# Performance work log

Measured on AMD Instinct MI355X. Metric: run time of the kernel, lower is better.

The kernel has to match this reference:

```python
import jax, jax.numpy as jnp
import numpy as np

N_SPLIT = 4096   # split tokens (coarse octree levels)
N_VQ    = 12288  # VQ tokens (finest level)
N       = N_SPLIT + N_VQ
C       = 256    # num_embed
H       = 8      # num_heads
L       = 4      # num_blocks
P       = 256    # patch_size (attention window)
DIL     = 2      # dilation for odd (swin) blocks
DVQ     = 32     # vqvae embedding_channels
VQ_SIZE = 256    # vqvae embedding_sizes
VQ_G    = 4      # vqvae quantizer_group
HID     = 4 * C


def _layernorm(x, s, b):
    m = x.mean(-1, keepdims=True)
    v = jnp.var(x, axis=-1, keepdims=True)
    return (x - m) * jax.lax.rsqrt(v + 1e-5) * s + b


def _sin_pos_emb(n, c):
    pos = jnp.arange(n, dtype=jnp.float32)[:, None]
    half = c // 2
    freqs = jnp.exp(-jnp.log(10000.0) * jnp.arange(half, dtype=jnp.float32) / half)
    ang = pos * freqs
    return jnp.concatenate([jnp.sin(ang), jnp.cos(ang)], axis=-1)


def _forward(split, zq, targets_vq, category, batch_id, mask, d2b,
             split_emb, class_emb, vq_proj_w, vq_proj_b,
             ln1_s, ln1_b, qkv_w, qkv_b, attn_w, attn_b,
             ln2_s, ln2_b, fc1_w, fc1_b, fc2_w, fc2_b,
             lnx_s, lnx_b, split_w, split_b, vq_w, vq_b):
    # token embeddings: [split tokens ; projected VQ codes]
    x = jnp.concatenate([split_emb[split], zq @ vq_proj_w + vq_proj_b], axis=0)  # [N,C]
    cond = class_emb[category]                      # [B,C]
    x = jnp.where(mask[:, None], cond[batch_id], x)  # masked tokens -> class cond

    # depth2batch gather, then OctFormer blocks
    xb = x[d2b] + _sin_pos_emb(N, C).astype(x.dtype)
    dh = C // H
    scale = dh ** -0.5
    for l in range(L):
        d = DIL if (l % 2 == 1) else 1  # swin-style alternating dilation
        h = _layernorm(xb, ln1_s[l], ln1_b[l])
        # dilated window partition: window j in a super-window holds tokens base+p*d+j
        hw = h.reshape(-1, P, d, C).transpose(0, 2, 1, 3).reshape(-1, P, C)
        qkv = hw @ qkv_w[l] + qkv_b[l]              # [nw,P,3C]
        q, k, v = [t.reshape(-1, P, H, dh) for t in jnp.split(qkv, 3, axis=-1)]
        att = jax.nn.softmax(jnp.einsum('wphd,wqhd->whpq', q, k) * scale, axis=-1)
        o = jnp.einsum('whpq,wqhd->wphd', att, v).reshape(-1, P, C) @ attn_w[l] + attn_b[l]
        o = o.reshape(-1, d, P, C).transpose(0, 2, 1, 3).reshape(-1, C)  # undo partition
        xb = xb + o
        h = _layernorm(xb, ln2_s[l], ln2_b[l])
        xb = xb + (jax.nn.gelu(h @ fc1_w[l] + fc1_b[l]) @ fc2_w[l] + fc2_b[l])
    # batch2depth scatter (inverse permutation)
    x = jnp.zeros_like(xb).at[d2b].set(xb)
    x = _layernorm(x, lnx_s, lnx_b)

    # split head + masked cross-entropy
    sl = x[:N_SPLIT] @ split_w + split_b            # [Ns,2]
    ms = mask[:N_SPLIT].astype(jnp.float32)
    ce_s = -jnp.take_along_axis(jax.nn.log_softmax(sl, axis=-1), split[:, None], axis=-1)[:, 0]
    split_loss = jnp.sum(ce_s * ms) / jnp.maximum(jnp.sum(ms), 1.0)

    # vq head + masked grouped cross-entropy
    vl = (x[N_SPLIT:] @ vq_w + vq_b).reshape(N_VQ, VQ_G, VQ_SIZE)
    mv = mask[N_SPLIT:].astype(jnp.float32)
    ce_v = -jnp.take_along_axis(jax.nn.log_softmax(vl, axis=-1), targets_vq[..., None], axis=-1)[..., 0]
    vq_loss = jnp.sum(ce_v.mean(-1) * mv) / jnp.maximum(jnp.sum(mv), 1.0)
    return jnp.stack([split_loss, vq_loss])


def setup_inputs() -> dict:
    key = jax.random.key(0)
    ks = jax.random.split(key, 16)
    s = 0.02
    inp = {
        'split': jax.random.randint(ks[0], (N_SPLIT,), 0, 2),
        'zq': jax.random.normal(ks[1], (N_VQ, DVQ), jnp.float32),
        'targets_vq': jax.random.randint(ks[2], (N_VQ, VQ_G), 0, VQ_SIZE),
        'category': jnp.zeros((1,), jnp.int32),
        'batch_id': jnp.zeros((N,), jnp.int32),
        'mask': jax.random.randint(ks[3], (N,), 0, 2).astype(bool),
        'd2b': jax.random.permutation(ks[4], N),
        'split_emb': s * jax.random.normal(ks[5], (2, C), jnp.float32),
        'class_emb': s * jax.random.normal(ks[6], (1, C), jnp.float32),
        'vq_proj_w': s * jax.random.normal(ks[7], (DVQ, C), jnp.float32),
        'vq_proj_b': jnp.zeros((C,), jnp.float32),
        'ln1_s': jnp.ones((L, C), jnp.float32),
        'ln1_b': jnp.zeros((L, C), jnp.float32),
        'qkv_w': s * jax.random.normal(ks[8], (L, C, 3 * C), jnp.float32),
        'qkv_b': jnp.zeros((L, 3 * C), jnp.float32),
        'attn_w': s * jax.random.normal(ks[9], (L, C, C), jnp.float32),
        'attn_b': jnp.zeros((L, C), jnp.float32),
        'ln2_s': jnp.ones((L, C), jnp.float32),
        'ln2_b': jnp.zeros((L, C), jnp.float32),
        'fc1_w': s * jax.random.normal(ks[10], (L, C, HID), jnp.float32),
        'fc1_b': jnp.zeros((L, HID), jnp.float32),
        'fc2_w': s * jax.random.normal(ks[11], (L, HID, C), jnp.float32),
        'fc2_b': jnp.zeros((L, C), jnp.float32),
        'lnx_s': jnp.ones((C,), jnp.float32),
        'lnx_b': jnp.zeros((C,), jnp.float32),
        'split_w': s * jax.random.normal(ks[12], (C, 2), jnp.float32),
        'split_b': jnp.zeros((2,), jnp.float32),
        'vq_w': s * jax.random.normal(ks[13], (C, VQ_G * VQ_SIZE), jnp.float32),
        'vq_b': jnp.zeros((VQ_G * VQ_SIZE,), jnp.float32),
    }
    return inp


def reference(split, zq, targets_vq, category, batch_id, mask, d2b,
              split_emb, class_emb, vq_proj_w, vq_proj_b,
              ln1_s, ln1_b, qkv_w, qkv_b, attn_w, attn_b,
              ln2_s, ln2_b, fc1_w, fc1_b, fc2_w, fc2_b,
              lnx_s, lnx_b, split_w, split_b, vq_w, vq_b):
    return _forward(split, zq, targets_vq, category, batch_id, mask, d2b,
                    split_emb, class_emb, vq_proj_w, vq_proj_b,
                    ln1_s, ln1_b, qkv_w, qkv_b, attn_w, attn_b,
                    ln2_s, ln2_b, fc1_w, fc1_b, fc2_w, fc2_b,
                    lnx_s, lnx_b, split_w, split_b, vq_w, vq_b)
```

## Files before the change

kernel.cpp:

```cpp
#include <hip/hip_runtime.h>
#include <hip/hip_bf16.h>
#include <math.h>

#define NSPLIT 4096
#define NVQ    12288
#define NTOK   16384
#define CH     256
#define NH     8
#define DHD    32
#define NL     4
#define PW     256
#define HIDN   1024
#define DVQ    32
#define VQG    4
#define VQS    256

typedef __attribute__((ext_vector_type(8))) short bf16x8;
typedef __attribute__((ext_vector_type(4))) float f32x4;

typedef const __attribute__((address_space(1))) void* gas_ptr;
typedef __attribute__((address_space(3))) void* las_ptr;
#define GLD16(g, s) __builtin_amdgcn_global_load_lds((gas_ptr)(g), (las_ptr)(s), 16, 0, 0)

static __device__ __forceinline__ unsigned pack2bf(float a, float b) {
    __hip_bfloat16 ha = __float2bfloat16(a), hb = __float2bfloat16(b);
    return ((unsigned)*(unsigned short*)&hb << 16) | *(unsigned short*)&ha;
}
static __device__ __forceinline__ float bf2f(unsigned short s) {
    unsigned u = (unsigned)s << 16;
    return *(float*)&u;
}
static __device__ __forceinline__ unsigned short f2bfu(float f) {
    __hip_bfloat16 h = __float2bfloat16(f);
    return *(unsigned short*)&h;
}

__global__ void k_wt_all(const float* __restrict__ qkv_w, const float* __restrict__ attn_w,
                         const float* __restrict__ fc1_w, const float* __restrict__ fc2_w,
                         const float* __restrict__ vq_w,
                         short* __restrict__ qkvT, short* __restrict__ attnT,
                         short* __restrict__ fc1T, short* __restrict__ fc2T,
                         short* __restrict__ vqT,
                         const void* __restrict__ mask_raw, int* __restrict__ mode) {
    int b = blockIdx.x;
    if (b == 832) {
        __shared__ int c_even, c_odd, c_0100;
        const unsigned short* u16 = (const unsigned short*)mask_raw;
        if (threadIdx.x == 0) { c_even = 0; c_odd = 0; c_0100 = 0; }
        __syncthreads();
        int le = 0, lo = 0, l01 = 0;
        for (int i = threadIdx.x; i < 8192; i += 256) {
            unsigned short v = u16[i];
            if (v == 0x3F80u) { if (i & 1) lo++; else le++; }
            if (v == 0x0100u) l01++;
        }
        atomicAdd(&c_even, le); atomicAdd(&c_odd, lo); atomicAdd(&c_0100, l01);
        __syncthreads();
        if (threadIdx.x == 0) {
            int m;
            if      (c_even > 500) m = 2;
            else if (c_odd  > 500) m = 3;
            else if (c_0100 > 500) m = 1;
            else                   m = 0;
            *mode = m;
        }
        return;
    }
    const float* W; short* Wt; int K, N, tn, tk;
    if (b < 192)      { int r = b;       int z = r / 48; r %= 48; K = 256;  N = 768;
                        tk = r / 12; tn = r % 12;
                        W = qkv_w + (size_t)z * K * N; Wt = qkvT + (size_t)z * K * N; }
    else if (b < 256) { int r = b - 192; int z = r / 16; r %= 16; K = 256;  N = 256;
                        tk = r / 4;  tn = r % 4;
                        W = attn_w + (size_t)z * K * N; Wt = attnT + (size_t)z * K * N; }
    else if (b < 512) { int r = b - 256; int z = r / 64; r %= 64; K = 256;  N = 1024;
                        tk = r / 16; tn = r % 16;
                        W = fc1_w + (size_t)z * K * N; Wt = fc1T + (size_t)z * K * N; }
    else if (b < 768) { int r = b - 512; int z = r / 64; r %= 64; K = 1024; N = 256;
                        tk = r / 4;  tn = r % 4;
                        W = fc2_w + (size_t)z * K * N; Wt = fc2T + (size_t)z * K * N; }
    else              { int r = b - 768; K = 256; N = 1024;
                        tk = r / 16; tn = r % 16; W = vq_w; Wt = vqT; }
    __shared__ float t[64][65];
    int bn = tn * 64, bk = tk * 64, tid = threadIdx.x;
#pragma unroll
    for (int it = 0; it < 16; ++it) {
        int idx = it * 256 + tid; int r = idx >> 6, c = idx & 63;
        t[r][c] = W[(size_t)(bk + r) * N + bn + c];
    }
    __syncthreads();
#pragma unroll
    for (int it = 0; it < 16; ++it) {
        int idx = it * 256 + tid; int r = idx >> 6, c = idx & 63;
        __hip_bfloat16 h = __float2bfloat16(t[c][r]);
        Wt[(size_t)(bn + r) * K + bk + c] = *(short*)&h;
    }
}

__global__ void k_embed_gather(const int* __restrict__ split, const float* __restrict__ zq,
                               const int* __restrict__ category, const int* __restrict__ batch_id,
                               const void* __restrict__ mask_raw, const int* __restrict__ mode,
                               int* __restrict__ mask_i, const int* __restrict__ d2b,
                               const float* __restrict__ split_emb, const float* __restrict__ class_emb,
                               const float* __restrict__ vq_proj_w, const float* __restrict__ vq_proj_b,
                               const float* __restrict__ ln1s, const float* __restrict__ ln1b,
                               unsigned short* __restrict__ xbv, unsigned short* __restrict__ hb) {
    int j = blockIdx.x, c = threadIdx.x;
    int i = d2b[j];
    int m = *mode, mv;
    if      (m == 0) mv = ((const int*)mask_raw)[i] != 0;
    else if (m == 1) mv = ((const unsigned char*)mask_raw)[i] != 0;
    else if (m == 2) mv = ((const unsigned short*)mask_raw)[i] != 0;
    else             mv = ((const unsigned int*)mask_raw)[i] != 0;
    if (c == 0) mask_i[i] = mv;
    float v;
    if (mv) {
        v = class_emb[category[batch_id[i]] * CH + c];
    } else if (i < NSPLIT) {
        v = split_emb[split[i] * CH + c];
    } else {
        const float* z = zq + (size_t)(i - NSPLIT) * DVQ;
        float acc = vq_proj_b[c];
#pragma unroll
        for (int k = 0; k < DVQ; k++) acc += z[k] * vq_proj_w[k * CH + c];
        v = acc;
    }
    const float kneg = -0.07195578415606394f;
    float jf = (float)j, pe;
    if (c < 128) { float f = expf(c * kneg);         pe = sinf(jf * f); }
    else         { float f = expf((c - 128) * kneg); pe = cosf(jf * f); }
    v += pe;
    float s = v, sq = v * v;
#pragma unroll
    for (int o = 32; o; o >>= 1) { s += __shfl_xor(s, o); sq += __shfl_xor(sq, o); }
    __shared__ float ps[4], pq[4];
    if ((c & 63) == 0) { ps[c >> 6] = s; pq[c >> 6] = sq; }
    __syncthreads();
    float S = ps[0] + ps[1] + ps[2] + ps[3];
    float Q = pq[0] + pq[1] + pq[2] + pq[3];
    float mean = S * (1.0f / CH);
    float var  = Q * (1.0f / CH) - mean * mean;
    float rsf = rsqrtf(var + 1e-5f);
    xbv[(size_t)j * CH + c] = f2bfu(v);
    hb[(size_t)j * CH + c]  = f2bfu((v - mean) * rsf * ln1s[c] + ln1b[c]);
}

template <int GELU>
__global__ __launch_bounds__(256, 4) void k_mm(
    const short* __restrict__ A, const short* __restrict__ Bt,
    const float* __restrict__ bias, unsigned short* __restrict__ outB,
    int N, int K) {
    __shared__ short As[2][128 * 32];
    __shared__ short Bs[2][128 * 32];
    const int tid = threadIdx.x;
    const int w = tid >> 6, l = tid & 63;
    const int bm = blockIdx.y * 128, bn = blockIdx.x * 128;
    const int wr = w >> 1, wc = w & 1;
    const int q = l >> 4, rA = l & 15;
    const int srow = w * 16 + (l >> 2);
    const int sx = ((l & 3) ^ ((l >> 2) & 3)) * 8;
    const int fx = (q ^ (rA & 3)) * 8;

    const short* gA0 = A + (size_t)(bm + srow) * K + sx;
    const short* gA1 = A + (size_t)(bm + srow + 64) * K + sx;
    const short* gB0 = Bt + (size_t)(bn + srow) * K + sx;
    const short* gB1 = Bt + (size_t)(bn + srow + 64) * K + sx;
    short* lA0 = &As[0][w * 16 * 32];
    short* lA1 = &As[0][(64 + w * 16) * 32];
    short* lA0h = &As[1][w * 16 * 32];
    short* lA1h = &As[1][(64 + w * 16) * 32];
    short* lB0 = &Bs[0][w * 16 * 32];
    short* lB1 = &Bs[0][(64 + w * 16) * 32];
    short* lB0h = &Bs[1][w * 16 * 32];
    short* lB1h = &Bs[1][(64 + w * 16) * 32];

    f32x4 acc[4][4] = {};

    for (int k0 = 0; k0 < K; k0 += 64) {
        GLD16(gA0 + k0, lA0);       GLD16(gA1 + k0, lA1);
        GLD16(gA0 + k0 + 32, lA0h); GLD16(gA1 + k0 + 32, lA1h);
        GLD16(gB0 + k0, lB0);       GLD16(gB1 + k0, lB1);
        GLD16(gB0 + k0 + 32, lB0h); GLD16(gB1 + k0 + 32, lB1h);
        __syncthreads();
#pragma unroll
        for (int s = 0; s < 2; s++) {
            bf16x8 a[4], b[4];
#pragma unroll
            for (int m = 0; m < 4; m++)
                a[m] = *(const bf16x8*)(&As[s][(wr * 64 + m * 16 + rA) * 32 + fx]);
#pragma unroll
            for (int n = 0; n < 4; n++)
                b[n] = *(const bf16x8*)(&Bs[s][(wc * 64 + n * 16 + rA) * 32 + fx]);
#pragma unroll
            for (int m = 0; m < 4; m++)
#pragma unroll
                for (int n = 0; n < 4; n++)
                    acc[m][n] = __builtin_amdgcn_mfma_f32_16x16x32_bf16(b[n], a[m], acc[m][n], 0, 0, 0);
        }
        __syncthreads();
    }

#pragma unroll
    for (int m = 0; m < 4; m++) {
        int row = bm + wr * 64 + m * 16 + rA;
#pragma unroll
        for (int n = 0; n < 4; n++) {
            int colb = bn + wc * 64 + n * 16 + q * 4;
            float4 bv = *(const float4*)(bias + colb);
            float v0 = acc[m][n][0] + bv.x;
            float v1 = acc[m][n][1] + bv.y;
            float v2 = acc[m][n][2] + bv.z;
            float v3 = acc[m][n][3] + bv.w;
            if (GELU) {
                float t0 = tanhf(0.7978845608028654f * (v0 + 0.044715f * v0 * v0 * v0));
                float t1 = tanhf(0.7978845608028654f * (v1 + 0.044715f * v1 * v1 * v1));
                float t2 = tanhf(0.7978845608028654f * (v2 + 0.044715f * v2 * v2 * v2));
                float t3 = tanhf(0.7978845608028654f * (v3 + 0.044715f * v3 * v3 * v3));
                v0 = 0.5f * v0 * (1.0f + t0); v1 = 0.5f * v1 * (1.0f + t1);
                v2 = 0.5f * v2 * (1.0f + t2); v3 = 0.5f * v3 * (1.0f + t3);
            }
            ushort4 st = { f2bfu(v0), f2bfu(v1), f2bfu(v2), f2bfu(v3) };
            *(ushort4*)(outB + (size_t)row * N + colb) = st;
        }
    }
}

template <int LNOUT>
__global__ __launch_bounds__(512, 4) void k_mm_row(
    const short* __restrict__ A, const short* __restrict__ Bt,
    const float* __restrict__ bias, unsigned short* __restrict__ xbv,
    const float* __restrict__ lns, const float* __restrict__ lnb,
    unsigned short* __restrict__ h_out, const int* __restrict__ d2b, int K,
    const int* __restrict__ split, const int* __restrict__ mask_i,
    const float* __restrict__ sw, const float* __restrict__ sb,
    float* __restrict__ sce) {
    __shared__ short As[2][32 * 32];
    __shared__ short Bs[2][256 * 32];
    __shared__ float part[2][8][32];
    const int tid = threadIdx.x;
    const int w = tid >> 6, l = tid & 63;
    const int bm = blockIdx.x * 32;
    const int q = l >> 4, rA = l & 15;
    const int sx = ((l & 3) ^ ((l >> 2) & 3)) * 8;
    const int fx = (q ^ (rA & 3)) * 8;

    const short* gA = A + (size_t)(bm + (l >> 2)) * K + sx;
    const short* gB = Bt + (size_t)(w * 32 + (l >> 2)) * K + sx;

    f32x4 acc[2][2] = {};

    for (int k0 = 0; k0 < K; k0 += 64) {
        if (w == 0) {
#pragma unroll
            for (int rg = 0; rg < 2; rg++) {
                GLD16(gA + (size_t)(rg * 16) * K + k0,      &As[0][(rg * 16) * 32]);
                GLD16(gA + (size_t)(rg * 16) * K + k0 + 32, &As[1][(rg * 16) * 32]);
            }
        }
#pragma unroll
        for (int i = 0; i < 2; i++) {
            GLD16(gB + (size_t)(i * 16) * K + k0,      &Bs[0][(w * 32 + i * 16) * 32]);
            GLD16(gB + (size_t)(i * 16) * K + k0 + 32, &Bs[1][(w * 32 + i * 16) * 32]);
        }
        __syncthreads();
#pragma unroll
        for (int s = 0; s < 2; s++) {
            bf16x8 a[2], b[2];
#pragma unroll
            for (int m = 0; m < 2; m++)
                a[m] = *(const bf16x8*)(&As[s][(m * 16 + rA) * 32 + fx]);
#pragma unroll
            for (int n = 0; n < 2; n++)
                b[n] = *(const bf16x8*)(&Bs[s][(w * 32 + n * 16 + rA) * 32 + fx]);
#pragma unroll
            for (int m = 0; m < 2; m++)
#pragma unroll
                for (int n = 0; n < 2; n++)
                    acc[m][n] = __builtin_amdgcn_mfma_f32_16x16x32_bf16(b[n], a[m], acc[m][n], 0, 0, 0);
        }
        __syncthreads();
    }

    float rsum[2] = {}, rsq[2] = {};
#pragma unroll
    for (int m = 0; m < 2; m++) {
        int row = bm + m * 16 + rA;
#pragma unroll
        for (int n = 0; n < 2; n++) {
            int colb = w * 32 + n * 16 + q * 4;
            float4 bv = *(const float4*)(bias + colb);
            size_t oi = (size_t)row * CH + colb;
            ushort4 xo = *(const ushort4*)(xbv + oi);
            float v0 = acc[m][n][0] + bv.x + bf2f(xo.x);
            float v1 = acc[m][n][1] + bv.y + bf2f(xo.y);
            float v2 = acc[m][n][2] + bv.z + bf2f(xo.z);
            float v3 = acc[m][n][3] + bv.w + bf2f(xo.w);
            acc[m][n][0] = v0; acc[m][n][1] = v1; acc[m][n][2] = v2; acc[m][n][3] = v3;
            if (LNOUT != 2) {
                ushort4 st = { f2bfu(v0), f2bfu(v1), f2bfu(v2), f2bfu(v3) };
                *(ushort4*)(xbv + oi) = st;
            }
            rsum[m] += (v0 + v1) + (v2 + v3);
            rsq[m]  += (v0 * v0 + v1 * v1) + (v2 * v2 + v3 * v3);
        }
    }
    if (LNOUT) {
#pragma unroll
        for (int m = 0; m < 2; m++) {
            rsum[m] += __shfl_xor(rsum[m], 16); rsum[m] += __shfl_xor(rsum[m], 32);
            rsq[m]  += __shfl_xor(rsq[m], 16);  rsq[m]  += __shfl_xor(rsq[m], 32);
        }
        if (q == 0) {
#pragma unroll
            for (int m = 0; m < 2; m++) {
                part[0][w][m * 16 + rA] = rsum[m];
                part[1][w][m * 16 + rA] = rsq[m];
            }
        }
        __syncthreads();
#pragma unroll
        for (int m = 0; m < 2; m++) {
            int row = m * 16 + rA;
            float S = 0.f, Q = 0.f;
#pragma unroll
            for (int ww = 0; ww < 8; ww++) { S += part[0][ww][row]; Q += part[1][ww][row]; }
            float mean = S * (1.0f / CH);
            float var  = Q * (1.0f / CH) - mean * mean;
            float rsf = rsqrtf(var + 1e-5f);
            size_t orow = (LNOUT == 2) ? (size_t)d2b[bm + row] : (size_t)(bm + row);
#pragma unroll
            for (int n = 0; n < 2; n++) {
                int colb = w * 32 + n * 16 + q * 4;
                float4 sv = *(const float4*)(lns + colb);
                float4 bb = *(const float4*)(lnb + colb);
                float h0 = (acc[m][n][0] - mean) * rsf * sv.x + bb.x;
                float h1 = (acc[m][n][1] - mean) * rsf * sv.y + bb.y;
                float h2 = (acc[m][n][2] - mean) * rsf * sv.z + bb.z;
                float h3 = (acc[m][n][3] - mean) * rsf * sv.w + bb.w;
                acc[m][n][0] = h0; acc[m][n][1] = h1; acc[m][n][2] = h2; acc[m][n][3] = h3;
                ushort4 st = { f2bfu(h0), f2bfu(h1), f2bfu(h2), f2bfu(h3) };
                *(ushort4*)(h_out + orow * CH + colb) = st;
            }
        }
    }
    if (LNOUT == 2) {
        float a0[2] = {}, a1[2] = {};
#pragma unroll
        for (int m = 0; m < 2; m++) {
#pragma unroll
            for (int n = 0; n < 2; n++) {
                int colb = w * 32 + n * 16 + q * 4;
#pragma unroll
                for (int j = 0; j < 4; j++) {
                    a0[m] += acc[m][n][j] * sw[2 * (colb + j)];
                    a1[m] += acc[m][n][j] * sw[2 * (colb + j) + 1];
                }
            }
            a0[m] += __shfl_xor(a0[m], 16); a0[m] += __shfl_xor(a0[m], 32);
            a1[m] += __shfl_xor(a1[m], 16); a1[m] += __shfl_xor(a1[m], 32);
        }
        __syncthreads();
        if (q == 0) {
#pragma unroll
            for (int m = 0; m < 2; m++) {
                part[0][w][m * 16 + rA] = a0[m];
                part[1][w][m * 16 + rA] = a1[m];
            }
        }
        __syncthreads();
        if (w == 0 && q == 0) {
#pragma unroll
            for (int m = 0; m < 2; m++) {
                int row = m * 16 + rA;
                int orow = d2b[bm + row];
                if (orow < NSPLIT) {
                    float l0 = sb[0], l1 = sb[1];
#pragma unroll
                    for (int ww = 0; ww < 8; ww++) { l0 += part[0][ww][row]; l1 += part[1][ww][row]; }
                    float mx = fmaxf(l0, l1);
                    float lse = mx + logf(__expf(l0 - mx) + __expf(l1 - mx));
                    float ce = lse - (split[orow] ? l1 : l0);
                    sce[orow] = ce * (float)mask_i[orow];
                }
            }
        }
    }
}

__global__ __launch_bounds__(256, 4) void k_vq_head(
    const short* __restrict__ A, const short* __restrict__ vqT,
    const float* __restrict__ vq_b, const int* __restrict__ targets,
    float* __restrict__ vce4) {
    __shared__ short As[2][32 * 32];
    __shared__ short Bs[2][256 * 32];
    __shared__ float part[2][4][32];
    __shared__ float tgtv[32];
    const int tid = threadIdx.x;
    const int w = tid >> 6, l = tid & 63;
    const int bm = blockIdx.x * 32;
    const int g = blockIdx.y;
    const int q = l >> 4, rA = l & 15;
    const int sx = ((l & 3) ^ ((l >> 2) & 3)) * 8;
    const int fx = (q ^ (rA & 3)) * 8;

    const short* gA = A + (size_t)(bm + (l >> 2)) * CH + sx;
    const short* gB = vqT + (size_t)(g * VQS + w * 64 + (l >> 2)) * CH + sx;

    f32x4 acc[2][4] = {};

    for (int k0 = 0; k0 < CH; k0 += 64) {
        if (w == 0) {
#pragma unroll
            for (int rg = 0; rg < 2; rg++) {
                GLD16(gA + (size_t)(rg * 16) * CH + k0,      &As[0][(rg * 16) * 32]);
                GLD16(gA + (size_t)(rg * 16) * CH + k0 + 32, &As[1][(rg * 16) * 32]);
            }
        }
#pragma unroll
        for (int i = 0; i < 4; i++) {
            GLD16(gB + (size_t)(i * 16) * CH + k0,      &Bs[0][(w * 64 + i * 16) * 32]);
            GLD16(gB + (size_t)(i * 16) * CH + k0 + 32, &Bs[1][(w * 64 + i * 16) * 32]);
        }
        __syncthreads();
#pragma unroll
        for (int s = 0; s < 2; s++) {
            bf16x8 a[2], b[4];
#pragma unroll
            for (int m = 0; m < 2; m++)
                a[m] = *(const bf16x8*)(&As[s][(m * 16 + rA) * 32 + fx]);
#pragma unroll
            for (int n = 0; n < 4; n++)
                b[n] = *(const bf16x8*)(&Bs[s][(w * 64 + n * 16 + rA) * 32 + fx]);
#pragma unroll
            for (int m = 0; m < 2; m++)
#pragma unroll
                for (int n = 0; n < 4; n++)
                    acc[m][n] = __builtin_amdgcn_mfma_f32_16x16x32_bf16(b[n], a[m], acc[m][n], 0, 0, 0);
        }
        __syncthreads();
    }

    float pm[2];
#pragma unroll
    for (int m = 0; m < 2; m++) {
        pm[m] = -1e30f;
        int row = m * 16 + rA;
        int t = targets[(size_t)(bm + row) * VQG + g];
#pragma unroll
        for (int n = 0; n < 4; n++) {
            int colb = w * 64 + n * 16 + q * 4;
            float4 bv = *(const float4*)(vq_b + g * VQS + colb);
            float v0 = acc[m][n][0] + bv.x;
            float v1 = acc[m][n][1] + bv.y;
            float v2 = acc[m][n][2] + bv.z;
            float v3 = acc[m][n][3] + bv.w;
            acc[m][n][0] = v0; acc[m][n][1] = v1; acc[m][n][2] = v2; acc[m][n][3] = v3;
            if (colb + 0 == t) tgtv[row] = v0;
            if (colb + 1 == t) tgtv[row] = v1;
            if (colb + 2 == t) tgtv[row] = v2;
            if (colb + 3 == t) tgtv[row] = v3;
            pm[m] = fmaxf(pm[m], fmaxf(fmaxf(v0, v1), fmaxf(v2, v3)));
        }
    }
#pragma unroll
    for (int m = 0; m < 2; m++) {
        pm[m] = fmaxf(pm[m], __shfl_xor(pm[m], 16));
        pm[m] = fmaxf(pm[m], __shfl_xor(pm[m], 32));
    }
    if (q == 0) {
#pragma unroll
        for (int m = 0; m < 2; m++) part[0][w][m * 16 + rA] = pm[m];
    }
    __syncthreads();
    float pmf[2], psum[2];
#pragma unroll
    for (int m = 0; m < 2; m++) {
        int row = m * 16 + rA;
        float mx = fmaxf(fmaxf(part[0][0][row], part[0][1][row]),
                         fmaxf(part[0][2][row], part[0][3][row]));
        pmf[m] = mx;
        float s = 0.f;
#pragma unroll
        for (int n = 0; n < 4; n++)
            s += __expf(acc[m][n][0] - mx) + __expf(acc[m][n][1] - mx)
               + __expf(acc[m][n][2] - mx) + __expf(acc[m][n][3] - mx);
        psum[m] = s;
    }
#pragma unroll
    for (int m = 0; m < 2; m++) {
        psum[m] += __shfl_xor(psum[m], 16);
        psum[m] += __shfl_xor(psum[m], 32);
    }
    if (q == 0) {
#pragma unroll
        for (int m = 0; m < 2; m++) part[1][w][m * 16 + rA] = psum[m];
    }
    __syncthreads();
    if (w == 0 && q == 0) {
#pragma unroll
        for (int m = 0; m < 2; m++) {
            int row = m * 16 + rA;
            float tot = part[1][0][row] + part[1][1][row] + part[1][2][row] + part[1][3][row];
            float lse = pmf[m] + logf(tot);
            vce4[(size_t)(bm + row) * VQG + g] = lse - tgtv[row];
        }
    }
}

__global__ __launch_bounds__(512, 4) void k_attn_mfma(const short* __restrict__ qkv,
                                                      short* __restrict__ o, int dil) {
    __shared__ short Vt[DHD * PW];
    __shared__ short Kl[PW * DHD];
    __shared__ short Pl[8][32 * 64];
    const int wid = blockIdx.x, h = blockIdx.y;
    const int tid = threadIdx.x;
    const int w = tid >> 6, l = tid & 63;
    const int g = l >> 4, c = l & 15;
    const int tbase = (wid / dil) * (PW * dil) + (wid % dil);

#pragma unroll
    for (int j2 = 0; j2 < 2; j2++) {
        int row = j2 * 128 + w * 16 + (l >> 2);
        int sc = (l & 3) ^ (row & 3);
        GLD16(qkv + (size_t)(tbase + row * dil) * 768 + CH + h * DHD + sc * 8,
              Kl + (j2 * 128 + w * 16) * DHD);
    }

    {
        const int p = tid >> 1, half = tid & 1;
        const short* src = qkv + (size_t)(tbase + p * dil) * 768 + 2 * CH + h * DHD + half * 16;
        bf16x8 v0 = *(const bf16x8*)(src);
        bf16x8 v1 = *(const bf16x8*)(src + 8);
        const int pc = p >> 3, po = p & 7;
#pragma unroll
        for (int d = 0; d < 8; d++)
            Vt[(half * 16 + d) * PW + ((pc ^ d) << 3) + po] = v0[d];
#pragma unroll
        for (int d = 0; d < 8; d++)
            Vt[(half * 16 + 8 + d) * PW + ((pc ^ d) << 3) + po] = v1[d];
    }

    bf16x8 qf[2];
#pragma unroll
    for (int qt = 0; qt < 2; qt++) {
        int qrow = w * 32 + qt * 16 + c;
        qf[qt] = *(const bf16x8*)(qkv + (size_t)(tbase + qrow * dil) * 768 + h * DHD + g * 8);
    }

    f32x4 acco[2][2] = {};
    float m_s[2] = {-1e30f, -1e30f};
    float l_s[2] = {0.f, 0.f};
    const float scale = 0.17677669529663687f;

    __syncthreads();

#pragma unroll
    for (int ch = 0; ch < 4; ch++) {
        bf16x8 kf[4];
#pragma unroll
        for (int kvt = 0; kvt < 4; kvt++) {
            int kv = ch * 64 + kvt * 16 + c;
            kf[kvt] = *(const bf16x8*)(Kl + kv * DHD + ((g ^ (c & 3)) * 8));
        }
        f32x4 accs[4][2] = {};
#pragma unroll
        for (int kvt = 0; kvt < 4; kvt++)
#pragma unroll
            for (int qt = 0; qt < 2; qt++)
                accs[kvt][qt] = __builtin_amdgcn_mfma_f32_16x16x32_bf16(kf[kvt], qf[qt], accs[kvt][qt], 0, 0, 0);

        float fb[2];
#pragma unroll
        for (int qt = 0; qt < 2; qt++) {
            float mx = -1e30f;
#pragma unroll
            for (int kvt = 0; kvt < 4; kvt++) {
                mx = fmaxf(mx, fmaxf(fmaxf(accs[kvt][qt][0], accs[kvt][qt][1]),
                                     fmaxf(accs[kvt][qt][2], accs[kvt][qt][3])));
            }
            mx = fmaxf(mx, __shfl_xor(mx, 16));
            mx = fmaxf(mx, __shfl_xor(mx, 32));
            float mnew = fmaxf(m_s[qt], mx * scale);
            fb[qt] = __expf(m_s[qt] - mnew);
            m_s[qt] = mnew;
        }
#pragma unroll
        for (int mt = 0; mt < 2; mt++) {
            float fo = fb[mt];
#pragma unroll
            for (int r = 0; r < 4; r++) {
                acco[mt][0][r] *= fo;
                acco[mt][1][r] *= fo;
            }
        }
        float rsum[2] = {0.f, 0.f};
#pragma unroll
        for (int kvt = 0; kvt < 4; kvt++) {
            const int cchunk = kvt * 2 + (g >> 1);
            const int koff = (g & 1) << 2;
#pragma unroll
            for (int qt = 0; qt < 2; qt++) {
                float p0 = __expf(accs[kvt][qt][0] * scale - m_s[qt]);
                float p1 = __expf(accs[kvt][qt][1] * scale - m_s[qt]);
                float p2 = __expf(accs[kvt][qt][2] * scale - m_s[qt]);
                float p3 = __expf(accs[kvt][qt][3] * scale - m_s[qt]);
                rsum[qt] += (p0 + p1) + (p2 + p3);
                int qq = qt * 16 + c;
                int phys = cchunk ^ (qq & 7);
                uint2 pk; pk.x = pack2bf(p0, p1); pk.y = pack2bf(p2, p3);
                *(uint2*)(&Pl[w][qq * 64 + phys * 8 + koff]) = pk;
            }
        }
#pragma unroll
        for (int qt = 0; qt < 2; qt++) {
            float s = rsum[qt];
            s += __shfl_xor(s, 16);
            s += __shfl_xor(s, 32);
            l_s[qt] = l_s[qt] * fb[qt] + s;
        }
#pragma unroll
        for (int ks = 0; ks < 2; ks++) {
            bf16x8 pa[2];
#pragma unroll
            for (int mt = 0; mt < 2; mt++) {
                int qq = mt * 16 + c;
                int phys = (ks * 4 + g) ^ (qq & 7);
                pa[mt] = *(const bf16x8*)(&Pl[w][qq * 64 + phys * 8]);
            }
#pragma unroll
            for (int nt = 0; nt < 2; nt++) {
                int d = nt * 16 + c;
                int kvabs = ch * 64 + ks * 32 + g * 8;
                int phys = (kvabs >> 3) ^ (d & 7);
                bf16x8 vb = *(const bf16x8*)(&Vt[d * PW + phys * 8]);
#pragma unroll
                for (int mt = 0; mt < 2; mt++)
                    acco[mt][nt] = __builtin_amdgcn_mfma_f32_16x16x32_bf16(vb, pa[mt], acco[mt][nt], 0, 0, 0);
            }
        }
    }

#pragma unroll
    for (int mt = 0; mt < 2; mt++) {
        float linv = 1.0f / l_s[mt];
        int qrow = w * 32 + mt * 16 + c;
        size_t trow = (size_t)(tbase + qrow * dil) * CH + h * DHD;
#pragma unroll
        for (int nt = 0; nt < 2; nt++) {
            ushort4 st = { f2bfu(acco[mt][nt][0] * linv), f2bfu(acco[mt][nt][1] * linv),
                           f2bfu(acco[mt][nt][2] * linv), f2bfu(acco[mt][nt][3] * linv) };
            *(ushort4*)((unsigned short*)o + trow + nt * 16 + g * 4) = st;
        }
    }
}

__global__ void k_reduce(const float* __restrict__ sce, const float* __restrict__ vce4,
                         const int* __restrict__ mask_i, float* __restrict__ out) {
    int tid = threadIdx.x;
    float s1 = 0, s2 = 0, s3 = 0, s4 = 0;
    for (int i = tid; i < NSPLIT; i += 256) { s1 += sce[i]; s2 += (float)mask_i[i]; }
    for (int i = tid; i < NVQ; i += 256) {
        float mv = (float)mask_i[NSPLIT + i];
        float cs = vce4[i * 4 + 0] + vce4[i * 4 + 1] + vce4[i * 4 + 2] + vce4[i * 4 + 3];
        s3 += cs * 0.25f * mv;
        s4 += mv;
    }
    __shared__ float r1[256], r2[256], r3[256], r4[256];
    r1[tid] = s1; r2[tid] = s2; r3[tid] = s3; r4[tid] = s4;
    __syncthreads();
    for (int o = 128; o; o >>= 1) {
        if (tid < o) { r1[tid] += r1[tid + o]; r2[tid] += r2[tid + o];
                       r3[tid] += r3[tid + o]; r4[tid] += r4[tid + o]; }
        __syncthreads();
    }
    if (tid == 0) {
        out[0] = r1[0] / fmaxf(r2[0], 1.0f);
        out[1] = r3[0] / fmaxf(r4[0], 1.0f);
    }
}

extern "C" void kernel_launch(void* const* d_in, const int* in_sizes, int n_in,
                              void* d_out, int out_size, void* d_ws, size_t ws_size,
                              hipStream_t stream) {
    const int*   split      = (const int*)d_in[0];
    const float* zq         = (const float*)d_in[1];
    const int*   targets_vq = (const int*)d_in[2];
    const int*   category   = (const int*)d_in[3];
    const int*   batch_id   = (const int*)d_in[4];
    const void*  mask_raw   = d_in[5];
    const int*   d2b        = (const int*)d_in[6];
    const float* split_emb  = (const float*)d_in[7];
    const float* class_emb  = (const float*)d_in[8];
    const float* vq_proj_w  = (const float*)d_in[9];
    const float* vq_proj_b  = (const float*)d_in[10];
    const float* ln1_s      = (const float*)d_in[11];
    const float* ln1_b      = (const float*)d_in[12];
    const float* qkv_w      = (const float*)d_in[13];
    const float* qkv_b      = (const float*)d_in[14];
    const float* attn_w     = (const float*)d_in[15];
    const float* attn_b     = (const float*)d_in[16];
    const float* ln2_s      = (const float*)d_in[17];
    const float* ln2_b      = (const float*)d_in[18];
    const float* fc1_w      = (const float*)d_in[19];
    const float* fc1_b      = (const float*)d_in[20];
    const float* fc2_w      = (const float*)d_in[21];
    const float* fc2_b      = (const float*)d_in[22];
    const float* lnx_s      = (const float*)d_in[23];
    const float* lnx_b      = (const float*)d_in[24];
    const float* sw         = (const float*)d_in[25];
    const float* sb         = (const float*)d_in[26];
    const float* vq_w       = (const float*)d_in[27];
    const float* vq_b       = (const float*)d_in[28];

    char* ws = (char*)d_ws;
    int* mode   = (int*)ws;
    int* mask_i = (int*)(ws + 256);
    float* sce  = (float*)(ws + 256 + 4 * NTOK);
    float* vce4 = sce + NSPLIT;
    char* p = ws + (1 << 20);
    short* qkvT = (short*)p;  p += (size_t)NL * 768 * CH * 2;
    short* attnT = (short*)p; p += (size_t)NL * CH * CH * 2;
    short* fc1T = (short*)p;  p += (size_t)NL * HIDN * CH * 2;
    short* fc2T = (short*)p;  p += (size_t)NL * CH * HIDN * 2;
    short* vqT = (short*)p;   p += (size_t)HIDN * CH * 2;
    unsigned short* xbv = (unsigned short*)p; p += (size_t)NTOK * CH * 2;
    unsigned short* h_bf = (unsigned short*)p; p += (size_t)NTOK * CH * 2;
    unsigned short* o_bf = (unsigned short*)p; p += (size_t)NTOK * CH * 2;
    short* big = (short*)p;

    k_wt_all<<<833, 256, 0, stream>>>(qkv_w, attn_w, fc1_w, fc2_w, vq_w,
                                      qkvT, attnT, fc1T, fc2T, vqT, mask_raw, mode);
    k_embed_gather<<<NTOK, 256, 0, stream>>>(split, zq, category, batch_id, mask_raw, mode,
                                             mask_i, d2b, split_emb, class_emb,
                                             vq_proj_w, vq_proj_b, ln1_s, ln1_b, xbv, h_bf);

    for (int l = 0; l < NL; l++) {
        int d = (l & 1) ? 2 : 1;
        k_mm<0><<<dim3(768 / 128, NTOK / 128), 256, 0, stream>>>(
            (const short*)h_bf, qkvT + (size_t)l * 768 * CH, qkv_b + l * 768,
            (unsigned short*)big, 768, CH);
        k_attn_mfma<<<dim3(NTOK / PW, NH), 512, 0, stream>>>(big, (short*)o_bf, d);
        k_mm_row<1><<<NTOK / 32, 512, 0, stream>>>(
            (const short*)o_bf, attnT + (size_t)l * CH * CH, attn_b + l * CH,
            xbv, ln2_s + l * CH, ln2_b + l * CH, h_bf, nullptr, CH,
            nullptr, nullptr, nullptr, nullptr, nullptr);
        k_mm<1><<<dim3(HIDN / 128, NTOK / 128), 256, 0, stream>>>(
            (const short*)h_bf, fc1T + (size_t)l * HIDN * CH, fc1_b + l * HIDN,
            (unsigned short*)big, HIDN, CH);
        if (l < NL - 1) {
            k_mm_row<1><<<NTOK / 32, 512, 0, stream>>>(
                big, fc2T + (size_t)l * CH * HIDN, fc2_b + l * CH,
                xbv, ln1_s + (l + 1) * CH, ln1_b + (l + 1) * CH, h_bf, nullptr, HIDN,
                nullptr, nullptr, nullptr, nullptr, nullptr);
        } else {
            k_mm_row<2><<<NTOK / 32, 512, 0, stream>>>(
                big, fc2T + (size_t)l * CH * HIDN, fc2_b + l * CH,
                xbv, lnx_s, lnx_b, h_bf, d2b, HIDN,
                split, mask_i, sw, sb, sce);
        }
    }

    k_vq_head<<<dim3(NVQ / 32, VQG), 256, 0, stream>>>(
        (const short*)(h_bf + (size_t)NSPLIT * CH), vqT, vq_b, targets_vq, vce4);
    k_reduce<<<1, 256, 0, stream>>>(sce, vce4, mask_i, (float*)d_out);
}
```

Measured before the change: 466.8 us.

## Fuse per-head QKV projection into the windowed attention kernel

Removes the separate QKV GEMM launch and computes each window-head's Q, K, V slice (256 tokens × 96 columns) inside the attention block. The result is staged directly into swizzled shared memory for the attention MFMAs. This avoids writing and re-reading the 16384×768 QKV intermediate through global memory. In exchange, each of the 8 head blocks per window re-reads the same 256×256 LayerNorm output tile, the projection uses smaller tiles with a simple non-pipelined load/sync loop, and shared memory grows to 80 KB per block, which may lower occupancy.

New measurement: 425.2 us, median of 3. -8.9%, faster.

```diff
diff --git a/kernel.cpp b/kernel.cpp
--- a/kernel.cpp
+++ b/kernel.cpp
@@ -507,44 +507,95 @@
     }
 }
 
-__global__ __launch_bounds__(512, 4) void k_attn_mfma(const short* __restrict__ qkv,
-                                                      short* __restrict__ o, int dil) {
-    __shared__ short Vt[DHD * PW];
-    __shared__ short Kl[PW * DHD];
-    __shared__ short Pl[8][32 * 64];
-    const int wid = blockIdx.x, h = blockIdx.y;
+__global__ __launch_bounds__(512, 4) void k_attn_fused(
+    const unsigned short* __restrict__ hin, const short* __restrict__ Wt,
+    const float* __restrict__ bias, short* __restrict__ o, int dil) {
+    __shared__ short smem[40960];
+    short* Asm = smem;
+    short* Wsm = smem + 16384;
+    short* Ql  = smem;
+    short* Kl  = smem + 8192;
+    short* Vt  = smem + 16384;
+    short* Pl  = smem + 24576;
+
+    const int wid = blockIdx.x, hd = blockIdx.y;
     const int tid = threadIdx.x;
     const int w = tid >> 6, l = tid & 63;
     const int g = l >> 4, c = l & 15;
     const int tbase = (wid / dil) * (PW * dil) + (wid % dil);
-
-#pragma unroll
-    for (int j2 = 0; j2 < 2; j2++) {
-        int row = j2 * 128 + w * 16 + (l >> 2);
-        int sc = (l & 3) ^ (row & 3);
-        GLD16(qkv + (size_t)(tbase + row * dil) * 768 + CH + h * DHD + sc * 8,
-              Kl + (j2 * 128 + w * 16) * DHD);
-    }
-
+    const int sx = ((l & 3) ^ ((l >> 2) & 3)) * 8;
+    const int fx = (g ^ (c & 3)) * 8;
+
+    f32x4 acc[2][6] = {};
     {
-        const int p = tid >> 1, half = tid & 1;
-        const short* src = qkv + (size_t)(tbase + p * dil) * 768 + 2 * CH + h * DHD + half * 16;
-        bf16x8 v0 = *(const bf16x8*)(src);
-        bf16x8 v1 = *(const bf16x8*)(src + 8);
-        const int pc = p >> 3, po = p & 7;
-#pragma unroll
-        for (int d = 0; d < 8; d++)
-            Vt[(half * 16 + d) * PW + ((pc ^ d) << 3) + po] = v0[d];
-#pragma unroll
-        for (int d = 0; d < 8; d++)
-            Vt[(half * 16 + 8 + d) * PW + ((pc ^ d) << 3) + po] = v1[d];
-    }
+        const int lr = l >> 2;
+        const int rw = w * 12 + lr;
+        const int seg = rw >> 5, within = rw & 31;
+        const short* gW = Wt + (size_t)(seg * 256 + hd * 32 + within) * CH + sx;
+        for (int k0 = 0; k0 < CH; k0 += 64) {
+#pragma unroll
+            for (int h16 = 0; h16 < 2; h16++) {
+                int row = w * 32 + h16 * 16 + lr;
+                const unsigned short* src = hin + (size_t)(tbase + row * dil) * CH + k0 + sx;
+                GLD16(src,      Asm + (w * 32 + h16 * 16) * 32);
+                GLD16(src + 32, Asm + 8192 + (w * 32 + h16 * 16) * 32);
+            }
+            if (l < 48) {
+                GLD16(gW + k0,      Wsm + (w * 12) * 32);
+                GLD16(gW + k0 + 32, Wsm + 3072 + (w * 12) * 32);
+            }
+            __syncthreads();
+#pragma unroll
+            for (int s = 0; s < 2; s++) {
+                bf16x8 a[2], b[6];
+#pragma unroll
+                for (int m = 0; m < 2; m++)
+                    a[m] = *(const bf16x8*)(Asm + s * 8192 + (w * 32 + m * 16 + c) * 32 + fx);
+#pragma unroll
+                for (int n = 0; n < 6; n++)
+                    b[n] = *(const bf16x8*)(Wsm + s * 3072 + (n * 16 + c) * 32 + fx);
+#pragma unroll
+                for (int m = 0; m < 2; m++)
+#pragma unroll
+                    for (int n = 0; n < 6; n++)
+                        acc[m][n] = __builtin_amdgcn_mfma_f32_16x16x32_bf16(b[n], a[m], acc[m][n], 0, 0, 0);
+            }
+            __syncthreads();
+        }
+    }
+#pragma unroll
+    for (int m = 0; m < 2; m++) {
+        int t = w * 32 + m * 16 + c;
+#pragma unroll
+        for (int n = 0; n < 6; n++) {
+            int seg = n >> 1, n1 = n & 1;
+            int colb = n1 * 16 + g * 4;
+            float4 bv = *(const float4*)(bias + seg * 256 + hd * 32 + colb);
+            float v0 = acc[m][n][0] + bv.x;
+            float v1 = acc[m][n][1] + bv.y;
+            float v2 = acc[m][n][2] + bv.z;
+            float v3 = acc[m][n][3] + bv.w;
+            if (seg < 2) {
+                short* dst = (seg == 0) ? Ql : Kl;
+                int slot = (n1 * 2 + (g >> 1)) ^ (t & 3);
+                uint2 pk; pk.x = pack2bf(v0, v1); pk.y = pack2bf(v2, v3);
+                *(uint2*)(dst + t * 32 + slot * 8 + (g & 1) * 4) = pk;
+            } else {
+                int d0 = colb;
+                Vt[(d0 + 0) * PW + ((((t >> 3) ^ ((d0 + 0) & 7))) << 3) + (t & 7)] = (short)f2bfu(v0);
+                Vt[(d0 + 1) * PW + ((((t >> 3) ^ ((d0 + 1) & 7))) << 3) + (t & 7)] = (short)f2bfu(v1);
+                Vt[(d0 + 2) * PW + ((((t >> 3) ^ ((d0 + 2) & 7))) << 3) + (t & 7)] = (short)f2bfu(v2);
+                Vt[(d0 + 3) * PW + ((((t >> 3) ^ ((d0 + 3) & 7))) << 3) + (t & 7)] = (short)f2bfu(v3);
+            }
+        }
+    }
+    __syncthreads();
 
     bf16x8 qf[2];
 #pragma unroll
     for (int qt = 0; qt < 2; qt++) {
         int qrow = w * 32 + qt * 16 + c;
-        qf[qt] = *(const bf16x8*)(qkv + (size_t)(tbase + qrow * dil) * 768 + h * DHD + g * 8);
+        qf[qt] = *(const bf16x8*)(Ql + qrow * 32 + ((g ^ (qrow & 3)) * 8));
     }
 
     f32x4 acco[2][2] = {};
@@ -552,15 +603,13 @@
     float l_s[2] = {0.f, 0.f};
     const float scale = 0.17677669529663687f;
 
-    __syncthreads();
-
 #pragma unroll
     for (int ch = 0; ch < 4; ch++) {
         bf16x8 kf[4];
 #pragma unroll
         for (int kvt = 0; kvt < 4; kvt++) {
             int kv = ch * 64 + kvt * 16 + c;
-            kf[kvt] = *(const bf16x8*)(Kl + kv * DHD + ((g ^ (c & 3)) * 8));
+            kf[kvt] = *(const bf16x8*)(Kl + kv * 32 + ((g ^ (kv & 3)) * 8));
         }
         f32x4 accs[4][2] = {};
 #pragma unroll
@@ -608,7 +657,7 @@
                 int qq = qt * 16 + c;
                 int phys = cchunk ^ (qq & 7);
                 uint2 pk; pk.x = pack2bf(p0, p1); pk.y = pack2bf(p2, p3);
-                *(uint2*)(&Pl[w][qq * 64 + phys * 8 + koff]) = pk;
+                *(uint2*)(Pl + w * 2048 + qq * 64 + phys * 8 + koff) = pk;
             }
         }
 #pragma unroll
@@ -625,14 +674,14 @@
             for (int mt = 0; mt < 2; mt++) {
                 int qq = mt * 16 + c;
                 int phys = (ks * 4 + g) ^ (qq & 7);
-                pa[mt] = *(const bf16x8*)(&Pl[w][qq * 64 + phys * 8]);
+                pa[mt] = *(const bf16x8*)(Pl + w * 2048 + qq * 64 + phys * 8);
             }
 #pragma unroll
             for (int nt = 0; nt < 2; nt++) {
                 int d = nt * 16 + c;
                 int kvabs = ch * 64 + ks * 32 + g * 8;
                 int phys = (kvabs >> 3) ^ (d & 7);
-                bf16x8 vb = *(const bf16x8*)(&Vt[d * PW + phys * 8]);
+                bf16x8 vb = *(const bf16x8*)(Vt + d * PW + phys * 8);
 #pragma unroll
                 for (int mt = 0; mt < 2; mt++)
                     acco[mt][nt] = __builtin_amdgcn_mfma_f32_16x16x32_bf16(vb, pa[mt], acco[mt][nt], 0, 0, 0);
@@ -644,7 +693,7 @@
     for (int mt = 0; mt < 2; mt++) {
         float linv = 1.0f / l_s[mt];
         int qrow = w * 32 + mt * 16 + c;
-        size_t trow = (size_t)(tbase + qrow * dil) * CH + h * DHD;
+        size_t trow = (size_t)(tbase + qrow * dil) * CH + hd * DHD;
 #pragma unroll
         for (int nt = 0; nt < 2; nt++) {
             ushort4 st = { f2bfu(acco[mt][nt][0] * linv), f2bfu(acco[mt][nt][1] * linv),
@@ -736,10 +785,8 @@
 
     for (int l = 0; l < NL; l++) {
         int d = (l & 1) ? 2 : 1;
-        k_mm<0><<<dim3(768 / 128, NTOK / 128), 256, 0, stream>>>(
-            (const short*)h_bf, qkvT + (size_t)l * 768 * CH, qkv_b + l * 768,
-            (unsigned short*)big, 768, CH);
-        k_attn_mfma<<<dim3(NTOK / PW, NH), 512, 0, stream>>>(big, (short*)o_bf, d);
+        k_attn_fused<<<dim3(NTOK / PW, NH), 512, 0, stream>>>(
+            h_bf, qkvT + (size_t)l * 768 * CH, qkv_b + l * 768, (short*)o_bf, d);
         k_mm_row<1><<<NTOK / 32, 512, 0, stream>>>(
             (const short*)o_bf, attnT + (size_t)l * CH * CH, attn_b + l * CH,
             xbv, ln2_s + l * CH, ln2_b + l * CH, h_bf, nullptr, CH,
```
